# Performance work log

Hardware: AMD Instinct MI355X
Metric: run time of the kernel (lower is better)

Reference implementation:

```python
import jax, jax.numpy as jnp
import numpy as np
import math

IN_FEATURES = 4096
OUT_FEATURES = 4096
TOKENS = 8192


def hydrate_weight(seed, out_features, in_features):
    """Deterministically synthesize the virtual weight matrix from the 64-bit seed.
    Mirrors nn.Linear's kaiming-uniform-style bound (1/sqrt(fan_in)) used by gmem_rs
    hydration; never stored as a parameter."""
    bound = 1.0 / math.sqrt(in_features)
    key = jax.random.key(seed)
    return jax.random.uniform(
        key, (out_features, in_features), dtype=jnp.float32,
        minval=-bound, maxval=bound)


def setup_inputs() -> dict:
    key = jax.random.key(0)
    kx, kb = jax.random.split(key)
    x = jax.random.normal(kx, (TOKENS, IN_FEATURES), dtype=jnp.float32)
    bound = 1.0 / math.sqrt(IN_FEATURES)
    bias = jax.random.uniform(kb, (OUT_FEATURES,), dtype=jnp.float32,
                              minval=-bound, maxval=bound)
    return {"x": x, "bias": bias, "seed": 1140071481}


def reference(x, bias, seed):
    # Hydrate weight on-the-fly from seed (zero-RAM virtual weight), then GEMM.
    W = hydrate_weight(seed, OUT_FEATURES, IN_FEATURES)  # [out, in]
    y = jnp.einsum('ti,oi->to', x, W)  # [tokens, out]
    return y + bias
```

## Files before the change

kernel.cpp:

```cpp
#include <hip/hip_runtime.h>
#include <hip/hip_bf16.h>
#include <stdint.h>

#define TOKENS 8192
#define NOUT   4096
#define KIN    4096

#define BM 256
#define BN 256
#define BK 64
#define NT (KIN / BK)

typedef __attribute__((ext_vector_type(8))) short bf16x8;
typedef __attribute__((ext_vector_type(4))) float f32x4;

__device__ __forceinline__ uint32_t rotl32(uint32_t x, int r) {
  return (x << r) | (x >> (32 - r));
}

__device__ __forceinline__ uint16_t f2bf_rne(float f) {
  uint32_t u = __float_as_uint(f);
  u += 0x7FFFu + ((u >> 16) & 1u);
  return (uint16_t)(u >> 16);
}

__device__ __forceinline__ void threefry2x32(uint32_t k0, uint32_t k1,
                                             uint32_t c0, uint32_t c1,
                                             uint32_t& o0, uint32_t& o1) {
  uint32_t ks2 = 0x1BD11BDAu ^ k0 ^ k1;
  uint32_t x0 = c0 + k0;
  uint32_t x1 = c1 + k1;
#define TFR(r) { x0 += x1; x1 = rotl32(x1, (r)); x1 ^= x0; }
  TFR(13) TFR(15) TFR(26) TFR(6)
  x0 += k1;  x1 += ks2 + 1u;
  TFR(17) TFR(29) TFR(16) TFR(24)
  x0 += ks2; x1 += k0 + 2u;
  TFR(13) TFR(15) TFR(26) TFR(6)
  x0 += k0;  x1 += k1 + 3u;
  TFR(17) TFR(29) TFR(16) TFR(24)
  x0 += k1;  x1 += ks2 + 4u;
  TFR(13) TFR(15) TFR(26) TFR(6)
  x0 += ks2; x1 += k0 + 5u;
#undef TFR
  o0 = x0; o1 = x1;
}

__global__ void prep_kernel(const float* __restrict__ x,
                            uint16_t* __restrict__ xb,
                            uint16_t* __restrict__ W,
                            const int* __restrict__ seed_ptr) {
  uint32_t b = blockIdx.x;
  if (b < 65536u) {
    uint32_t k1 = (uint32_t)(*seed_ptr);
    uint32_t j = b * 256u + threadIdx.x;
    uint32_t o0, o1;
    threefry2x32(0u, k1, 0u, j, o0, o1);
    uint32_t bits = o0 ^ o1;
    const float scale = 0.03125f;
    const float mn    = -0.015625f;
    float f = __uint_as_float((bits >> 9) | 0x3F800000u) - 1.0f;
    float v = fmaxf(mn, f * scale + mn);
    W[j] = f2bf_rne(v);
  } else {
    uint32_t base = ((b - 65536u) * 256u + threadIdx.x) * 8u;
    f32x4 a = *(const f32x4*)(x + base);
    f32x4 c = *(const f32x4*)(x + base + 4);
    union { uint16_t u[8]; bf16x8 v; } r;
    r.u[0] = f2bf_rne(a[0]); r.u[1] = f2bf_rne(a[1]);
    r.u[2] = f2bf_rne(a[2]); r.u[3] = f2bf_rne(a[3]);
    r.u[4] = f2bf_rne(c[0]); r.u[5] = f2bf_rne(c[1]);
    r.u[6] = f2bf_rne(c[2]); r.u[7] = f2bf_rne(c[3]);
    *(bf16x8*)(xb + base) = r.v;
  }
}

__global__ __launch_bounds__(512, 2)
void gemm_bias_kernel(const uint16_t* __restrict__ A,
                      const uint16_t* __restrict__ B,
                      const float* __restrict__ bias,
                      float* __restrict__ C) {
  __shared__ uint16_t smem[2][2][16384];

  const int nwgn = NOUT / BN;
  const int nwg  = (TOKENS / BM) * nwgn;
  int bid = blockIdx.x;
  int cpx = nwg >> 3;
  int swzb = (bid & 7) * cpx + (bid >> 3);
  int tm = (swzb / nwgn) * BM;
  int tn = (swzb % nwgn) * BN;

  const int t    = threadIdx.x;
  const int lane = t & 63;
  const int wid  = t >> 6;
  const int wm   = wid >> 2;
  const int wn   = wid & 3;
  const int fr   = lane & 15;
  const int fq   = lane >> 4;

  const int swzRd = (lane & 7) << 4;
  const int lsw   = ((lane & 7) ^ (lane >> 3)) << 4;

  f32x4 acc[8][4] = {};

  auto stageHalf = [&](int mat, int h, int kt, int buf) {
    const uint16_t* g = mat ? B : A;
    const int rb = (mat ? tn : tm) + h * 128 + wid * 16 + (lane >> 3);
    const char* src = (const char*)(g + (size_t)rb * KIN) + kt * 128 + lsw;
    char* dst = (char*)&smem[buf][mat][0] + h * 16384 + wid * 2048 + lane * 16;
#pragma unroll
    for (int q = 0; q < 2; ++q) {
      __builtin_amdgcn_global_load_lds(
          (const __attribute__((address_space(1))) void*)(src + (size_t)q * 8 * KIN * 2),
          (__attribute__((address_space(3))) void*)(dst + q * 1024),
          16, 0, 0);
    }
  };

#define VMW(N) asm volatile("s_waitcnt vmcnt(" #N ")" ::: "memory")
#define LKW(N) asm volatile("s_waitcnt lgkmcnt(" #N ")" ::: "memory")
#define SB0    __builtin_amdgcn_sched_barrier(0)
#define PRI(p) __builtin_amdgcn_s_setprio(p)

#define RD_A(BUFI, MH)                                                         \
    _Pragma("unroll")                                                          \
    for (int s_ = 0; s_ < 2; ++s_) {                                           \
      const int kb_ = (s_ << 6) | (fq << 4);                                   \
      _Pragma("unroll")                                                        \
      for (int i_ = 0; i_ < 4; ++i_)                                           \
        af[s_][i_] = *(const bf16x8*)((const char*)&smem[BUFI][0][0] +         \
            (wm * 64 + (MH) * 128 + i_ * 16 + fr) * 128 + (kb_ ^ swzRd));      \
    }

#define RD_B(BUFI, BV, NH)                                                     \
    _Pragma("unroll")                                                          \
    for (int s_ = 0; s_ < 2; ++s_) {                                           \
      const int kb_ = (s_ << 6) | (fq << 4);                                   \
      _Pragma("unroll")                                                        \
      for (int j_ = 0; j_ < 2; ++j_)                                           \
        BV[s_][j_] = *(const bf16x8*)((const char*)&smem[BUFI][1][0] +         \
            (wn * 32 + (NH) * 128 + j_ * 16 + fr) * 128 + (kb_ ^ swzRd));      \
    }

#define MF16(MH, NH, BV)                                                       \
    _Pragma("unroll")                                                          \
    for (int s_ = 0; s_ < 2; ++s_)                                             \
      _Pragma("unroll")                                                        \
      for (int i_ = 0; i_ < 4; ++i_)                                           \
        _Pragma("unroll")                                                      \
        for (int j_ = 0; j_ < 2; ++j_)                                         \
          acc[(MH) * 4 + i_][(NH) * 2 + j_] =                                  \
              __builtin_amdgcn_mfma_f32_16x16x32_bf16(                         \
                  af[s_][i_], BV[s_][j_], acc[(MH) * 4 + i_][(NH) * 2 + j_],   \
                  0, 0, 0);

#define KTILE(BUF, KT, MODE)                                                   \
  {                                                                            \
            \
    RD_A(BUF, 0) RD_B(BUF, bv0, 0)                                             \
    if ((MODE) <= 1) stageHalf(0, 1, (KT) + 1, (BUF) ^ 1);                     \
    __builtin_amdgcn_s_barrier();                                              \
    LKW(0); SB0; PRI(1); MF16(0, 0, bv0) PRI(0);                               \
                                       \
    RD_B(BUF, bv1, 1)                                                          \
    __builtin_amdgcn_s_barrier();                                              \
    LKW(0); SB0; PRI(1); MF16(0, 1, bv1) PRI(0);                               \
              \
    RD_A(BUF, 1)                                                               \
    if ((MODE) == 0) { stageHalf(0, 0, (KT) + 2, (BUF));                       \
                       stageHalf(1, 0, (KT) + 2, (BUF)); }                     \
    __builtin_amdgcn_s_barrier();                                              \
    LKW(0); SB0; PRI(1); MF16(1, 1, bv1) PRI(0);                               \
                      \
    if ((MODE) == 0) stageHalf(1, 1, (KT) + 2, (BUF));                         \
    if ((MODE) == 0) { VMW(6); } else if ((MODE) == 1) { VMW(0); }             \
    __builtin_amdgcn_s_barrier();                                              \
    SB0; PRI(1); MF16(1, 0, bv0) PRI(0);                                       \
  }

  bf16x8 af[2][4], bv0[2][2], bv1[2][2];

  stageHalf(0, 0, 0, 0); stageHalf(1, 0, 0, 0);
  stageHalf(0, 1, 0, 0); stageHalf(1, 1, 0, 0);
  VMW(4);
  stageHalf(0, 0, 1, 1); stageHalf(1, 0, 1, 1); stageHalf(1, 1, 1, 1);
  VMW(6);
  __builtin_amdgcn_s_barrier();

  for (int kt = 0; kt < NT - 2; kt += 2) {
    KTILE(0, kt, 0)
    KTILE(1, kt + 1, 0)
  }
  KTILE(0, 62, 1)
  KTILE(1, 63, 2)

#undef KTILE
#undef MF16
#undef RD_B
#undef RD_A
#undef PRI
#undef SB0
#undef LKW
#undef VMW

#pragma unroll
  for (int nj = 0; nj < 4; ++nj) {
    const int nh = nj >> 1, j = nj & 1;
    const int col = tn + wn * 32 + nh * 128 + j * 16 + fr;
    const float bvs = bias[col];
#pragma unroll
    for (int mi = 0; mi < 8; ++mi) {
      const int mh = mi >> 2, i = mi & 3;
      const int row0 = tm + wm * 64 + mh * 128 + i * 16 + fq * 4;
#pragma unroll
      for (int rr = 0; rr < 4; ++rr)
        C[(size_t)(row0 + rr) * NOUT + col] = acc[mi][nj][rr] + bvs;
    }
  }
}

extern "C" void kernel_launch(void* const* d_in, const int* in_sizes, int n_in,
                              void* d_out, int out_size, void* d_ws, size_t ws_size,
                              hipStream_t stream) {
  const float* x    = (const float*)d_in[0];
  const float* bias = (const float*)d_in[1];
  const int*   seed = (const int*)d_in[2];
  float* y = (float*)d_out;

  uint16_t* Wb = (uint16_t*)d_ws;
  uint16_t* Xb = Wb + (size_t)NOUT * KIN;

  prep_kernel<<<65536 + 16384, 256, 0, stream>>>(x, Xb, Wb, seed);

  const int grid = (TOKENS / BM) * (NOUT / BN);
  gemm_bias_kernel<<<grid, 512, 0, stream>>>(Xb, Wb, bias, y);
}
```

Before: 273.0 us.

## Split LDS fragment reads per k-substep with partial lgkmcnt waits; interleave prep blocks

The GEMM k-tile loop now reads LDS fragments in two k-substep halves and waits only for the first half (partial lgkmcnt) before issuing its MFMAs. The second half's loads can then overlap with compute instead of waiting for a full lgkmcnt(0). Separately, the prep kernel interleaves weight-hydration blocks with x-conversion blocks (4:1) so that memory-bound and ALU-bound work run at the same time on the GPU. The partial wait counts must match the exact issue order of the LDS loads, and the extra sched barriers limit what the compiler can reorder.

```diff
diff --git a/kernel.cpp b/kernel.cpp
--- a/kernel.cpp
+++ b/kernel.cpp
@@ -50,9 +50,10 @@
                             uint16_t* __restrict__ W,
                             const int* __restrict__ seed_ptr) {
   uint32_t b = blockIdx.x;
-  if (b < 65536u) {
+  uint32_t g = b / 5u, r = b % 5u;
+  if (r < 4u) {
     uint32_t k1 = (uint32_t)(*seed_ptr);
-    uint32_t j = b * 256u + threadIdx.x;
+    uint32_t j = (g * 4u + r) * 256u + threadIdx.x;
     uint32_t o0, o1;
     threefry2x32(0u, k1, 0u, j, o0, o1);
     uint32_t bits = o0 ^ o1;
@@ -62,15 +63,15 @@
     float v = fmaxf(mn, f * scale + mn);
     W[j] = f2bf_rne(v);
   } else {
-    uint32_t base = ((b - 65536u) * 256u + threadIdx.x) * 8u;
+    uint32_t base = (g * 256u + threadIdx.x) * 8u;
     f32x4 a = *(const f32x4*)(x + base);
     f32x4 c = *(const f32x4*)(x + base + 4);
-    union { uint16_t u[8]; bf16x8 v; } r;
-    r.u[0] = f2bf_rne(a[0]); r.u[1] = f2bf_rne(a[1]);
-    r.u[2] = f2bf_rne(a[2]); r.u[3] = f2bf_rne(a[3]);
-    r.u[4] = f2bf_rne(c[0]); r.u[5] = f2bf_rne(c[1]);
-    r.u[6] = f2bf_rne(c[2]); r.u[7] = f2bf_rne(c[3]);
-    *(bf16x8*)(xb + base) = r.v;
+    union { uint16_t u[8]; bf16x8 v; } rr;
+    rr.u[0] = f2bf_rne(a[0]); rr.u[1] = f2bf_rne(a[1]);
+    rr.u[2] = f2bf_rne(a[2]); rr.u[3] = f2bf_rne(a[3]);
+    rr.u[4] = f2bf_rne(c[0]); rr.u[5] = f2bf_rne(c[1]);
+    rr.u[6] = f2bf_rne(c[2]); rr.u[7] = f2bf_rne(c[3]);
+    *(bf16x8*)(xb + base) = rr.v;
   }
 }
 
@@ -121,60 +122,61 @@
 #define SB0    __builtin_amdgcn_sched_barrier(0)
 #define PRI(p) __builtin_amdgcn_s_setprio(p)
 
-#define RD_A(BUFI, MH)                                                         \
+#define RD_AS(BUFI, MH, S)                                                     \
     _Pragma("unroll")                                                          \
-    for (int s_ = 0; s_ < 2; ++s_) {                                           \
-      const int kb_ = (s_ << 6) | (fq << 4);                                   \
-      _Pragma("unroll")                                                        \
-      for (int i_ = 0; i_ < 4; ++i_)                                           \
-        af[s_][i_] = *(const bf16x8*)((const char*)&smem[BUFI][0][0] +         \
-            (wm * 64 + (MH) * 128 + i_ * 16 + fr) * 128 + (kb_ ^ swzRd));      \
-    }
-
-#define RD_B(BUFI, BV, NH)                                                     \
+    for (int i_ = 0; i_ < 4; ++i_)                                             \
+      af[S][i_] = *(const bf16x8*)((const char*)&smem[BUFI][0][0] +            \
+          (wm * 64 + (MH) * 128 + i_ * 16 + fr) * 128 +                        \
+          ((((S) << 6) | (fq << 4)) ^ swzRd));
+
+#define RD_BS(BUFI, BV, NH, S)                                                 \
     _Pragma("unroll")                                                          \
-    for (int s_ = 0; s_ < 2; ++s_) {                                           \
-      const int kb_ = (s_ << 6) | (fq << 4);                                   \
+    for (int j_ = 0; j_ < 2; ++j_)                                             \
+      BV[S][j_] = *(const bf16x8*)((const char*)&smem[BUFI][1][0] +            \
+          (wn * 32 + (NH) * 128 + j_ * 16 + fr) * 128 +                        \
+          ((((S) << 6) | (fq << 4)) ^ swzRd));
+
+#define MF8(MH, NH, BV, S)                                                     \
+    _Pragma("unroll")                                                          \
+    for (int i_ = 0; i_ < 4; ++i_)                                             \
       _Pragma("unroll")                                                        \
       for (int j_ = 0; j_ < 2; ++j_)                                           \
-        BV[s_][j_] = *(const bf16x8*)((const char*)&smem[BUFI][1][0] +         \
-            (wn * 32 + (NH) * 128 + j_ * 16 + fr) * 128 + (kb_ ^ swzRd));      \
-    }
-
-#define MF16(MH, NH, BV)                                                       \
-    _Pragma("unroll")                                                          \
-    for (int s_ = 0; s_ < 2; ++s_)                                             \
-      _Pragma("unroll")                                                        \
-      for (int i_ = 0; i_ < 4; ++i_)                                           \
-        _Pragma("unroll")                                                      \
-        for (int j_ = 0; j_ < 2; ++j_)                                         \
-          acc[(MH) * 4 + i_][(NH) * 2 + j_] =                                  \
-              __builtin_amdgcn_mfma_f32_16x16x32_bf16(                         \
-                  af[s_][i_], BV[s_][j_], acc[(MH) * 4 + i_][(NH) * 2 + j_],   \
-                  0, 0, 0);
+        acc[(MH) * 4 + i_][(NH) * 2 + j_] =                                    \
+            __builtin_amdgcn_mfma_f32_16x16x32_bf16(                           \
+                af[S][i_], BV[S][j_], acc[(MH) * 4 + i_][(NH) * 2 + j_],       \
+                0, 0, 0);
 
 #define KTILE(BUF, KT, MODE)                                                   \
   {                                                                            \
-            \
-    RD_A(BUF, 0) RD_B(BUF, bv0, 0)                                             \
+         \
+    RD_AS(BUF, 0, 0) RD_BS(BUF, bv0, 0, 0)                                     \
+    SB0;                                                                       \
+    RD_AS(BUF, 0, 1) RD_BS(BUF, bv0, 0, 1)                                     \
     if ((MODE) <= 1) stageHalf(0, 1, (KT) + 1, (BUF) ^ 1);                     \
     __builtin_amdgcn_s_barrier();                                              \
-    LKW(0); SB0; PRI(1); MF16(0, 0, bv0) PRI(0);                               \
-                                       \
-    RD_B(BUF, bv1, 1)                                                          \
-    __builtin_amdgcn_s_barrier();                                              \
-    LKW(0); SB0; PRI(1); MF16(0, 1, bv1) PRI(0);                               \
-              \
-    RD_A(BUF, 1)                                                               \
+    LKW(6); SB0; PRI(1); MF8(0, 0, bv0, 0)                                     \
+    LKW(0); SB0; MF8(0, 0, bv0, 1) PRI(0);                                     \
+                                                \
+    RD_BS(BUF, bv1, 1, 0)                                                      \
+    SB0;                                                                       \
+    RD_BS(BUF, bv1, 1, 1)                                                      \
+    __builtin_amdgcn_s_barrier();                                              \
+    LKW(2); SB0; PRI(1); MF8(0, 1, bv1, 0)                                     \
+    LKW(0); SB0; MF8(0, 1, bv1, 1) PRI(0);                                     \
+                       \
+    RD_AS(BUF, 1, 0)                                                           \
+    SB0;                                                                       \
+    RD_AS(BUF, 1, 1)                                                           \
     if ((MODE) == 0) { stageHalf(0, 0, (KT) + 2, (BUF));                       \
                        stageHalf(1, 0, (KT) + 2, (BUF)); }                     \
     __builtin_amdgcn_s_barrier();                                              \
-    LKW(0); SB0; PRI(1); MF16(1, 1, bv1) PRI(0);                               \
-                      \
+    LKW(4); SB0; PRI(1); MF8(1, 1, bv1, 0)                                     \
+    LKW(0); SB0; MF8(1, 1, bv1, 1) PRI(0);                                     \
+                   \
     if ((MODE) == 0) stageHalf(1, 1, (KT) + 2, (BUF));                         \
     if ((MODE) == 0) { VMW(6); } else if ((MODE) == 1) { VMW(0); }             \
     __builtin_amdgcn_s_barrier();                                              \
-    SB0; PRI(1); MF16(1, 0, bv0) PRI(0);                                       \
+    SB0; PRI(1); MF8(1, 0, bv0, 0) MF8(1, 0, bv0, 1) PRI(0);                   \
   }
 
   bf16x8 af[2][4], bv0[2][2], bv1[2][2];
@@ -194,9 +196,9 @@
   KTILE(1, 63, 2)
 
 #undef KTILE
-#undef MF16
-#undef RD_B
-#undef RD_A
+#undef MF8
+#undef RD_BS
+#undef RD_AS
 #undef PRI
 #undef SB0
 #undef LKW
@@ -229,7 +231,7 @@
   uint16_t* Wb = (uint16_t*)d_ws;
   uint16_t* Xb = Wb + (size_t)NOUT * KIN;
 
-  prep_kernel<<<65536 + 16384, 256, 0, stream>>>(x, Xb, Wb, seed);
+  prep_kernel<<<81920, 256, 0, stream>>>(x, Xb, Wb, seed);
 
   const int grid = (TOKENS / BM) * (NOUT / BN);
   gemm_bias_kernel<<<grid, 512, 0, stream>>>(Xb, Wb, bias, y);
```

Measured after the change: 252.0 us. 7.7% less time.
